# Kernel optimization log

Measured on AMD Instinct MI355X. Metric: run time of the kernel, lower is better.

The kernel has to match this reference:

```python
import jax, jax.numpy as jnp
import numpy as np

N_NODES = 100000
N_EDGES = 3200000
ALPHA = 0.1
ITERATIONS = 10


def setup_inputs() -> dict:
    key = jax.random.key(0)
    ks = jax.random.split(key, 7)
    features = jax.random.normal(ks[0], (N_NODES, 512), dtype=jnp.float32)
    W1 = jax.random.normal(ks[1], (512, 64), dtype=jnp.float32) * 0.05
    b1 = jax.random.normal(ks[2], (64,), dtype=jnp.float32) * 0.05
    W2 = jax.random.normal(ks[3], (64, 64), dtype=jnp.float32) * 0.05
    b2 = jax.random.normal(ks[4], (64,), dtype=jnp.float32) * 0.05
    edge_weights = jax.random.uniform(ks[5], (N_EDGES,), dtype=jnp.float32)
    edge_index = jax.random.randint(ks[6], (2, N_EDGES), 0, N_NODES, dtype=jnp.int64)
    return {"features": features, "W1": W1, "b1": b1, "W2": W2, "b2": b2,
            "edge_weights": edge_weights, "edge_index": edge_index}


def reference(features, W1, b1, W2, b2, edge_weights, edge_index):
    # dense MLP head (dropout disabled / eval mode)
    h = jax.nn.relu(features @ W1 + b1)          # [N, hidden]
    z = h @ W2 + b2                              # [N, labels]

    row, col = edge_index[0], edge_index[1]

    def step(p, _):
        # SpMM: out[row] += w * p[col]
        gathered = edge_weights[:, None] * p[col]                 # [E, labels]
        new = jax.ops.segment_sum(gathered, row, num_segments=N_NODES)
        p = (1.0 - ALPHA) * new + ALPHA * z
        return p, None

    p, _ = jax.lax.scan(step, z, None, length=ITERATIONS)
    return p
```

## Files before the change

kernel.cpp:

```cpp
#include <hip/hip_runtime.h>
#include <hip/hip_fp16.h>
#include <cmath>

#define N_NODES 100000
#define N_EDGES 3200000
#define ALPHA   0.1f
#define ITERS   10
#define NBUK    1024
#define RPB     98
#define CHUNK   8192
#define NCH     391

typedef __attribute__((ext_vector_type(8))) short short8;
typedef __attribute__((ext_vector_type(4))) float f32x4;

__device__ __forceinline__ short f2bf(float x) {
    union { float f; unsigned u; } v; v.f = x;
    unsigned r = v.u + 0x7fffu + ((v.u >> 16) & 1u);
    return (short)(r >> 16);
}

__global__ void prep_w(const float* __restrict__ W1, const float* __restrict__ W2,
                       short* __restrict__ W1t, short* __restrict__ W2t)
{
    int t = blockIdx.x * 256 + threadIdx.x;
    if (t < 512 * 64) { int k = t >> 6, c = t & 63; W1t[c * 512 + k] = f2bf(W1[t]); }
    if (t < 64 * 64)  { int k = t >> 6, c = t & 63; W2t[c * 64 + k]  = f2bf(W2[t]); }
}

__global__ __launch_bounds__(128) void mlp_mfma(
    const float* __restrict__ F, const short* __restrict__ W1t,
    const short* __restrict__ W2t, const float* __restrict__ b1,
    const float* __restrict__ b2, __half* __restrict__ q0)
{
    __shared__ short Ft[32 * 128];
    __shared__ short Ht[32 * 64];

    const int t  = threadIdx.x;
    const int l  = t & 63;
    const int wv = t >> 6;
    const int wr = wv * 16;
    const long base = (long)blockIdx.x * 32;

    const int sr = t >> 2;
    const int ck = (t & 3) * 32;

    float4 f0, f1, f2, f3, f4, f5, f6, f7;

#define LOAD_TILE(kt) do {                                                   \
    const float* p_ = F + (base + sr) * 512 + (kt) * 128 + ck;               \
    f0 = *(const float4*)(p_ +  0);  f1 = *(const float4*)(p_ +  4);         \
    f2 = *(const float4*)(p_ +  8);  f3 = *(const float4*)(p_ + 12);         \
    f4 = *(const float4*)(p_ + 16);  f5 = *(const float4*)(p_ + 20);         \
    f6 = *(const float4*)(p_ + 24);  f7 = *(const float4*)(p_ + 28);         \
} while (0)

#define STORE_PAIR(j2, fa, fb) do {                                          \
    int k_ = ck + (j2) * 8;                                                  \
    short8 s_ = { f2bf((fa).x), f2bf((fa).y), f2bf((fa).z), f2bf((fa).w),    \
                  f2bf((fb).x), f2bf((fb).y), f2bf((fb).z), f2bf((fb).w) };  \
    *(short8*)&Ft[(sr * 128 + k_) ^ ((sr & 7) << 3)] = s_;                   \
} while (0)

    LOAD_TILE(0);

    f32x4 acc[4] = {};
    for (int kt = 0; kt < 4; ++kt) {
        STORE_PAIR(0, f0, f1);
        STORE_PAIR(1, f2, f3);
        STORE_PAIR(2, f4, f5);
        STORE_PAIR(3, f6, f7);
        __syncthreads();
        if (kt < 3) LOAD_TILE(kt + 1);
#pragma unroll
        for (int kc = 0; kc < 4; ++kc) {
            int kb = kc * 32 + (l >> 4) * 8;
            int ar = wr + (l & 15);
            short8 a = *(const short8*)&Ft[(ar * 128 + kb) ^ ((ar & 7) << 3)];
#pragma unroll
            for (int n = 0; n < 4; ++n) {
                int bc = n * 16 + (l & 15);
                short8 b = *(const short8*)(W1t + bc * 512 + kt * 128 + kb);
                acc[n] = __builtin_amdgcn_mfma_f32_16x16x32_bf16(a, b, acc[n], 0, 0, 0);
            }
        }
        __syncthreads();
    }

#pragma unroll
    for (int n = 0; n < 4; ++n) {
        int col = n * 16 + (l & 15);
        float bv = b1[col];
#pragma unroll
        for (int i = 0; i < 4; ++i) {
            int row = wr + (l >> 4) * 4 + i;
            float hv = fmaxf(acc[n][i] + bv, 0.0f);
            Ht[(row * 64 + col) ^ ((row & 7) << 3)] = f2bf(hv);
        }
    }
    f32x4 acc2[4] = {};
#pragma unroll
    for (int kc = 0; kc < 2; ++kc) {
        int kb = kc * 32 + (l >> 4) * 8;
        int ar = wr + (l & 15);
        short8 a = *(const short8*)&Ht[(ar * 64 + kb) ^ ((ar & 7) << 3)];
#pragma unroll
        for (int n = 0; n < 4; ++n) {
            int bc = n * 16 + (l & 15);
            short8 b = *(const short8*)(W2t + bc * 64 + kb);
            acc2[n] = __builtin_amdgcn_mfma_f32_16x16x32_bf16(a, b, acc2[n], 0, 0, 0);
        }
    }
#pragma unroll
    for (int n = 0; n < 4; ++n) {
        int col = n * 16 + (l & 15);
        float bv = b2[col];
#pragma unroll
        for (int i = 0; i < 4; ++i) {
            long row = base + wr + (l >> 4) * 4 + i;
            q0[row * 64 + col] = __float2half(acc2[n][i] + bv);
        }
    }
#undef LOAD_TILE
#undef STORE_PAIR
}

__global__ __launch_bounds__(256) void bhist(const int* __restrict__ rows, int* __restrict__ gh)
{
    __shared__ int cnt[NBUK];
    for (int i = threadIdx.x; i < NBUK; i += 256) cnt[i] = 0;
    __syncthreads();
    int base = blockIdx.x * CHUNK;
    int end  = base + CHUNK; if (end > N_EDGES) end = N_EDGES;
    for (int i = base + threadIdx.x; i < end; i += 256)
        atomicAdd(&cnt[rows[i] / RPB], 1);
    __syncthreads();
    for (int i = threadIdx.x; i < NBUK; i += 256)
        gh[i * NCH + blockIdx.x] = cnt[i];
}

__global__ __launch_bounds__(512) void bscan(int* __restrict__ gh, int* __restrict__ btot)
{
    __shared__ int s[512];
    int k = blockIdx.x;
    int t = threadIdx.x;
    int v = (t < NCH) ? gh[k * NCH + t] : 0;
    s[t] = v;
    __syncthreads();
    for (int off = 1; off < 512; off <<= 1) {
        int x = (t >= off) ? s[t - off] : 0;
        __syncthreads();
        s[t] += x;
        __syncthreads();
    }
    if (t < NCH) gh[k * NCH + t] = s[t] - v;
    if (t == NCH - 1) btot[k] = s[t];
}

__global__ __launch_bounds__(1024) void scan_btot(const int* __restrict__ btot, int* __restrict__ bbase)
{
    __shared__ int s[1024];
    int t = threadIdx.x;
    int v = btot[t];
    s[t] = v;
    __syncthreads();
    for (int off = 1; off < 1024; off <<= 1) {
        int x = (t >= off) ? s[t - off] : 0;
        __syncthreads();
        s[t] += x;
        __syncthreads();
    }
    bbase[t] = s[t] - v;
}

__global__ __launch_bounds__(256) void bpart(const int* __restrict__ rows, const int* __restrict__ cols,
                                             const float* __restrict__ w, const int* __restrict__ gh,
                                             const int* __restrict__ bbase, uint2* __restrict__ stg)
{
    __shared__ int cur[NBUK];
    int blk = blockIdx.x;
    for (int i = threadIdx.x; i < NBUK; i += 256)
        cur[i] = bbase[i] + gh[i * NCH + blk];
    __syncthreads();
    int base = blk * CHUNK;
    int end  = base + CHUNK; if (end > N_EDGES) end = N_EDGES;
    for (int i = base + threadIdx.x; i < end; i += 256) {
        int r = rows[i];
        int b = r / RPB;
        int pos = atomicAdd(&cur[b], 1);
        float ws = w[i] * ((1.0f - ALPHA) / 16.0f);
        unsigned meta = (unsigned)cols[i] | ((unsigned)(r - b * RPB) << 17);
        stg[pos] = make_uint2(meta, __float_as_uint(ws));
    }
}

__global__ __launch_bounds__(256) void bucket_sort2(const int* __restrict__ bbase,
                                                    const uint2* __restrict__ stg,
                                                    unsigned long long* __restrict__ cw,
                                                    int* __restrict__ rowp)
{
    __shared__ int ldeg[RPB];
    __shared__ int lcur[RPB];
    __shared__ int sc[128];
    const int b = blockIdx.x;
    const int rowlo = b * RPB;
    if (rowlo >= N_NODES) return;
    int rowhi = rowlo + RPB; if (rowhi > N_NODES) rowhi = N_NODES;
    const int nrows = rowhi - rowlo;
    const int t = threadIdx.x;
    const int base = bbase[b];
    const int cnt = ((b + 1 < NBUK) ? bbase[b + 1] : N_EDGES) - base;

    if (t < RPB) ldeg[t] = 0;
    __syncthreads();
    for (int j = t; j < cnt; j += 256)
        atomicAdd(&ldeg[stg[base + j].x >> 17], 1);
    __syncthreads();
    int v = 0;
    if (t < 128) { v = (t < nrows) ? ldeg[t] : 0; sc[t] = v; }
    __syncthreads();
    for (int off = 1; off < 128; off <<= 1) {
        int x = (t < 128 && t >= off) ? sc[t - off] : 0;
        __syncthreads();
        if (t < 128) sc[t] += x;
        __syncthreads();
    }
    if (t < nrows) {
        int rp = base + sc[t] - v;
        rowp[rowlo + t] = rp;
        lcur[t] = rp;
    }
    if (t == 0 && rowhi == N_NODES) rowp[N_NODES] = base + cnt;
    __syncthreads();
    for (int j = t; j < cnt; j += 256) {
        uint2 rec = stg[base + j];
        int roff = rec.x >> 17;
        unsigned col = rec.x & 0x1FFFFu;
        int pos = atomicAdd(&lcur[roff], 1);
        cw[pos] = (unsigned long long)col | ((unsigned long long)rec.y << 32);
    }
}

template <int LAST>
__global__ __launch_bounds__(256) void spmm_kernel(
    const int* __restrict__ rowp, const unsigned long long* __restrict__ cw,
    const __half* __restrict__ qin, const __half* __restrict__ zh,
    float beta, float outscale,
    __half* __restrict__ qout, float* __restrict__ out)
{
    const int wid = blockIdx.x * 4 + (threadIdx.x >> 6);
    if (wid >= N_NODES) return;
    const int lane = threadIdx.x & 63;
    const int sub  = lane >> 3;
    const int l8   = lane & 7;

    const int start = rowp[wid];
    const int end   = rowp[wid + 1];

    uint4 zv = *(const uint4*)(zh + (long)wid * 64 + l8 * 8);

    float a0 = 0, a1 = 0, a2 = 0, a3 = 0, a4 = 0, a5 = 0, a6 = 0, a7 = 0;

#define ACC_EDGE(pc, v)                                                       \
    do {                                                                      \
        float ww_ = __uint_as_float((unsigned)((pc) >> 32));                  \
        float2 p_;                                                            \
        p_ = __half22float2(*(__half2*)&(v).x); a0 += ww_ * p_.x; a1 += ww_ * p_.y; \
        p_ = __half22float2(*(__half2*)&(v).y); a2 += ww_ * p_.x; a3 += ww_ * p_.y; \
        p_ = __half22float2(*(__half2*)&(v).z); a4 += ww_ * p_.x; a5 += ww_ * p_.y; \
        p_ = __half22float2(*(__half2*)&(v).w); a6 += ww_ * p_.x; a7 += ww_ * p_.y; \
    } while (0)

    int e = start + sub;
    for (; e + 8 < end; e += 16) {
        unsigned long long pc0 = cw[e];
        unsigned long long pc1 = cw[e + 8];
        uint4 v0 = *(const uint4*)(qin + (long)(unsigned)pc0 * 64 + l8 * 8);
        uint4 v1 = *(const uint4*)(qin + (long)(unsigned)pc1 * 64 + l8 * 8);
        ACC_EDGE(pc0, v0);
        ACC_EDGE(pc1, v1);
    }
    if (e < end) {
        unsigned long long pc = cw[e];
        uint4 v = *(const uint4*)(qin + (long)(unsigned)pc * 64 + l8 * 8);
        ACC_EDGE(pc, v);
    }
#undef ACC_EDGE

    a0 += __shfl_xor(a0, 8);  a1 += __shfl_xor(a1, 8);
    a2 += __shfl_xor(a2, 8);  a3 += __shfl_xor(a3, 8);
    a4 += __shfl_xor(a4, 8);  a5 += __shfl_xor(a5, 8);
    a6 += __shfl_xor(a6, 8);  a7 += __shfl_xor(a7, 8);
    a0 += __shfl_xor(a0, 16); a1 += __shfl_xor(a1, 16);
    a2 += __shfl_xor(a2, 16); a3 += __shfl_xor(a3, 16);
    a4 += __shfl_xor(a4, 16); a5 += __shfl_xor(a5, 16);
    a6 += __shfl_xor(a6, 16); a7 += __shfl_xor(a7, 16);
    a0 += __shfl_xor(a0, 32); a1 += __shfl_xor(a1, 32);
    a2 += __shfl_xor(a2, 32); a3 += __shfl_xor(a3, 32);
    a4 += __shfl_xor(a4, 32); a5 += __shfl_xor(a5, 32);
    a6 += __shfl_xor(a6, 32); a7 += __shfl_xor(a7, 32);

    if (lane < 8) {
        float2 z0 = __half22float2(*(__half2*)&zv.x);
        float2 z1 = __half22float2(*(__half2*)&zv.y);
        float2 z2 = __half22float2(*(__half2*)&zv.z);
        float2 z3 = __half22float2(*(__half2*)&zv.w);
        float o0 = a0 + beta * z0.x, o1 = a1 + beta * z0.y;
        float o2 = a2 + beta * z1.x, o3 = a3 + beta * z1.y;
        float o4 = a4 + beta * z2.x, o5 = a5 + beta * z2.y;
        float o6 = a6 + beta * z3.x, o7 = a7 + beta * z3.y;
        if (LAST) {
            float4 ra = { outscale * o0, outscale * o1, outscale * o2, outscale * o3 };
            float4 rb = { outscale * o4, outscale * o5, outscale * o6, outscale * o7 };
            *(float4*)(out + (long)wid * 64 + lane * 8)     = ra;
            *(float4*)(out + (long)wid * 64 + lane * 8 + 4) = rb;
        } else {
            __half2 h0 = __floats2half2_rn(o0, o1);
            __half2 h1 = __floats2half2_rn(o2, o3);
            __half2 h2 = __floats2half2_rn(o4, o5);
            __half2 h3 = __floats2half2_rn(o6, o7);
            uint4 pv = { *(unsigned*)&h0, *(unsigned*)&h1, *(unsigned*)&h2, *(unsigned*)&h3 };
            *(uint4*)(qout + (long)wid * 64 + lane * 8) = pv;
        }
    }
}

extern "C" void kernel_launch(void* const* d_in, const int* in_sizes, int n_in,
                              void* d_out, int out_size, void* d_ws, size_t ws_size,
                              hipStream_t stream)
{
    const float* features = (const float*)d_in[0];
    const float* W1 = (const float*)d_in[1];
    const float* b1 = (const float*)d_in[2];
    const float* W2 = (const float*)d_in[3];
    const float* b2 = (const float*)d_in[4];
    const float* ew = (const float*)d_in[5];
    const int*   ei = (const int*)d_in[6];
    const int* erow = ei;
    const int* ecol = ei + N_EDGES;
    float* out = (float*)d_out;

    char* ws = (char*)d_ws;
    size_t off = 0;
    auto alloc = [&](size_t bytes) {
        size_t c = off;
        off += (bytes + 255) & ~(size_t)255;
        return c;
    };
    __half* q0    = (__half*)(ws + alloc((size_t)N_NODES * 64 * 2));
    __half* qA    = (__half*)(ws + alloc((size_t)N_NODES * 64 * 2));
    __half* qB    = (__half*)(ws + alloc((size_t)N_NODES * 64 * 2));
    unsigned long long* cw = (unsigned long long*)(ws + alloc((size_t)N_EDGES * 8));
    uint2* stg    = (uint2*)(ws + alloc((size_t)N_EDGES * 8));
    int*   gh     = (int*)  (ws + alloc((size_t)NBUK * NCH * 4));
    short* W1t    = (short*)(ws + alloc((size_t)512 * 64 * 2));
    short* W2t    = (short*)(ws + alloc((size_t)64 * 64 * 2));
    int*   rowp   = (int*)  (ws + alloc((size_t)(N_NODES + 1) * 4));
    int*   btot   = (int*)  (ws + alloc((size_t)NBUK * 4));
    int*   bbase  = (int*)  (ws + alloc((size_t)NBUK * 4));
    (void)ws_size; (void)in_sizes; (void)n_in; (void)out_size;

    prep_w<<<128, 256, 0, stream>>>(W1, W2, W1t, W2t);
    mlp_mfma<<<N_NODES / 32, 128, 0, stream>>>(features, W1t, W2t, b1, b2, q0);

    bhist<<<NCH, 256, 0, stream>>>(erow, gh);
    bscan<<<NBUK, 512, 0, stream>>>(gh, btot);
    scan_btot<<<1, 1024, 0, stream>>>(btot, bbase);
    bpart<<<NCH, 256, 0, stream>>>(erow, ecol, ew, gh, bbase, stg);
    bucket_sort2<<<NBUK, 256, 0, stream>>>(bbase, stg, cw, rowp);

    const __half* qi = q0;
    for (int it = 1; it < ITERS; ++it) {
        __half* qo = (it & 1) ? qA : qB;
        float beta = (float)(0.1 / pow(16.0, (double)it));
        spmm_kernel<0><<<(N_NODES + 3) / 4, 256, 0, stream>>>(rowp, cw, qi, q0, beta, 1.0f, qo, nullptr);
        qi = qo;
    }
    float beta10 = (float)(0.1 / pow(16.0, 10.0));
    float osc    = (float)pow(16.0, 10.0);
    spmm_kernel<1><<<(N_NODES + 3) / 4, 256, 0, stream>>>(rowp, cw, qi, q0, beta10, osc, nullptr, out);
}
```

Baseline: 772.3 us.

## Split each row's edges into column-range chunks for gather locality

The bucket sort now orders each row's edges by one of four column ranges and stores per-row chunk lengths. The SpMM kernel walks the four segments in turn, so concurrent waves gather from similar regions of the feature matrix and cache reuse may improve. In exchange, each row pays four loop prologues and tails and an extra per-row metadata load.

```diff
diff --git a/kernel.cpp b/kernel.cpp
--- a/kernel.cpp
+++ b/kernel.cpp
@@ -10,6 +10,7 @@
 #define RPB     98
 #define CHUNK   8192
 #define NCH     391
+#define CCH     25000
 
 typedef __attribute__((ext_vector_type(8))) short short8;
 typedef __attribute__((ext_vector_type(4))) float f32x4;
@@ -194,13 +195,14 @@
     }
 }
 
-__global__ __launch_bounds__(256) void bucket_sort2(const int* __restrict__ bbase,
+__global__ __launch_bounds__(256) void bucket_sort3(const int* __restrict__ bbase,
                                                     const uint2* __restrict__ stg,
                                                     unsigned long long* __restrict__ cw,
-                                                    int* __restrict__ rowp)
-{
-    __shared__ int ldeg[RPB];
-    __shared__ int lcur[RPB];
+                                                    int* __restrict__ rowp,
+                                                    uint2* __restrict__ rowlen)
+{
+    __shared__ int ldeg[RPB * 4];
+    __shared__ int lcur[RPB * 4];
     __shared__ int sc[128];
     const int b = blockIdx.x;
     const int rowlo = b * RPB;
@@ -211,13 +213,20 @@
     const int base = bbase[b];
     const int cnt = ((b + 1 < NBUK) ? bbase[b + 1] : N_EDGES) - base;
 
-    if (t < RPB) ldeg[t] = 0;
-    __syncthreads();
-    for (int j = t; j < cnt; j += 256)
-        atomicAdd(&ldeg[stg[base + j].x >> 17], 1);
+    for (int i = t; i < RPB * 4; i += 256) ldeg[i] = 0;
+    __syncthreads();
+    for (int j = t; j < cnt; j += 256) {
+        unsigned x = stg[base + j].x;
+        int roff = x >> 17;
+        int ch = (int)((x & 0x1FFFFu) / CCH);
+        atomicAdd(&ldeg[roff * 4 + ch], 1);
+    }
     __syncthreads();
     int v = 0;
-    if (t < 128) { v = (t < nrows) ? ldeg[t] : 0; sc[t] = v; }
+    if (t < 128) {
+        v = (t < nrows) ? (ldeg[t * 4] + ldeg[t * 4 + 1] + ldeg[t * 4 + 2] + ldeg[t * 4 + 3]) : 0;
+        sc[t] = v;
+    }
     __syncthreads();
     for (int off = 1; off < 128; off <<= 1) {
         int x = (t < 128 && t >= off) ? sc[t - off] : 0;
@@ -228,7 +237,13 @@
     if (t < nrows) {
         int rp = base + sc[t] - v;
         rowp[rowlo + t] = rp;
-        lcur[t] = rp;
+        int c0 = ldeg[t * 4], c1 = ldeg[t * 4 + 1], c2 = ldeg[t * 4 + 2], c3 = ldeg[t * 4 + 3];
+        lcur[t * 4]     = rp;
+        lcur[t * 4 + 1] = rp + c0;
+        lcur[t * 4 + 2] = rp + c0 + c1;
+        lcur[t * 4 + 3] = rp + c0 + c1 + c2;
+        rowlen[rowlo + t] = make_uint2((unsigned)c0 | ((unsigned)c1 << 16),
+                                       (unsigned)c2 | ((unsigned)c3 << 16));
     }
     if (t == 0 && rowhi == N_NODES) rowp[N_NODES] = base + cnt;
     __syncthreads();
@@ -236,14 +251,16 @@
         uint2 rec = stg[base + j];
         int roff = rec.x >> 17;
         unsigned col = rec.x & 0x1FFFFu;
-        int pos = atomicAdd(&lcur[roff], 1);
+        int ch = (int)(col / CCH);
+        int pos = atomicAdd(&lcur[roff * 4 + ch], 1);
         cw[pos] = (unsigned long long)col | ((unsigned long long)rec.y << 32);
     }
 }
 
 template <int LAST>
 __global__ __launch_bounds__(256) void spmm_kernel(
-    const int* __restrict__ rowp, const unsigned long long* __restrict__ cw,
+    const int* __restrict__ rowp, const uint2* __restrict__ rowlen,
+    const unsigned long long* __restrict__ cw,
     const __half* __restrict__ qin, const __half* __restrict__ zh,
     float beta, float outscale,
     __half* __restrict__ qout, float* __restrict__ out)
@@ -255,7 +272,10 @@
     const int l8   = lane & 7;
 
     const int start = rowp[wid];
-    const int end   = rowp[wid + 1];
+    const uint2 rl  = rowlen[wid];
+    const int len0 = rl.x & 0xFFFF, len1 = rl.x >> 16;
+    const int len2 = rl.y & 0xFFFF, len3 = rl.y >> 16;
+    const int s1 = start + len0, s2 = s1 + len1, s3 = s2 + len2, e3 = s3 + len3;
 
     uint4 zv = *(const uint4*)(zh + (long)wid * 64 + l8 * 8);
 
@@ -271,20 +291,29 @@
         p_ = __half22float2(*(__half2*)&(v).w); a6 += ww_ * p_.x; a7 += ww_ * p_.y; \
     } while (0)
 
-    int e = start + sub;
-    for (; e + 8 < end; e += 16) {
-        unsigned long long pc0 = cw[e];
-        unsigned long long pc1 = cw[e + 8];
-        uint4 v0 = *(const uint4*)(qin + (long)(unsigned)pc0 * 64 + l8 * 8);
-        uint4 v1 = *(const uint4*)(qin + (long)(unsigned)pc1 * 64 + l8 * 8);
-        ACC_EDGE(pc0, v0);
-        ACC_EDGE(pc1, v1);
-    }
-    if (e < end) {
-        unsigned long long pc = cw[e];
-        uint4 v = *(const uint4*)(qin + (long)(unsigned)pc * 64 + l8 * 8);
-        ACC_EDGE(pc, v);
-    }
+#define DO_SEG(S, E)                                                          \
+    do {                                                                      \
+        int e = (S) + sub;                                                    \
+        for (; e + 8 < (E); e += 16) {                                        \
+            unsigned long long pc0 = cw[e];                                   \
+            unsigned long long pc1 = cw[e + 8];                               \
+            uint4 v0 = *(const uint4*)(qin + (long)(unsigned)pc0 * 64 + l8 * 8); \
+            uint4 v1 = *(const uint4*)(qin + (long)(unsigned)pc1 * 64 + l8 * 8); \
+            ACC_EDGE(pc0, v0);                                                \
+            ACC_EDGE(pc1, v1);                                                \
+        }                                                                     \
+        if (e < (E)) {                                                        \
+            unsigned long long pc = cw[e];                                    \
+            uint4 v = *(const uint4*)(qin + (long)(unsigned)pc * 64 + l8 * 8); \
+            ACC_EDGE(pc, v);                                                  \
+        }                                                                     \
+    } while (0)
+
+    DO_SEG(start, s1);
+    DO_SEG(s1, s2);
+    DO_SEG(s2, s3);
+    DO_SEG(s3, e3);
+#undef DO_SEG
 #undef ACC_EDGE
 
     a0 += __shfl_xor(a0, 8);  a1 += __shfl_xor(a1, 8);
@@ -356,6 +385,7 @@
     short* W1t    = (short*)(ws + alloc((size_t)512 * 64 * 2));
     short* W2t    = (short*)(ws + alloc((size_t)64 * 64 * 2));
     int*   rowp   = (int*)  (ws + alloc((size_t)(N_NODES + 1) * 4));
+    uint2* rowlen = (uint2*)(ws + alloc((size_t)N_NODES * 8));
     int*   btot   = (int*)  (ws + alloc((size_t)NBUK * 4));
     int*   bbase  = (int*)  (ws + alloc((size_t)NBUK * 4));
     (void)ws_size; (void)in_sizes; (void)n_in; (void)out_size;
@@ -367,16 +397,16 @@
     bscan<<<NBUK, 512, 0, stream>>>(gh, btot);
     scan_btot<<<1, 1024, 0, stream>>>(btot, bbase);
     bpart<<<NCH, 256, 0, stream>>>(erow, ecol, ew, gh, bbase, stg);
-    bucket_sort2<<<NBUK, 256, 0, stream>>>(bbase, stg, cw, rowp);
+    bucket_sort3<<<NBUK, 256, 0, stream>>>(bbase, stg, cw, rowp, rowlen);
 
     const __half* qi = q0;
     for (int it = 1; it < ITERS; ++it) {
         __half* qo = (it & 1) ? qA : qB;
         float beta = (float)(0.1 / pow(16.0, (double)it));
-        spmm_kernel<0><<<(N_NODES + 3) / 4, 256, 0, stream>>>(rowp, cw, qi, q0, beta, 1.0f, qo, nullptr);
+        spmm_kernel<0><<<(N_NODES + 3) / 4, 256, 0, stream>>>(rowp, rowlen, cw, qi, q0, beta, 1.0f, qo, nullptr);
         qi = qo;
     }
     float beta10 = (float)(0.1 / pow(16.0, 10.0));
     float osc    = (float)pow(16.0, 10.0);
-    spmm_kernel<1><<<(N_NODES + 3) / 4, 256, 0, stream>>>(rowp, cw, qi, q0, beta10, osc, nullptr, out);
-}
+    spmm_kernel<1><<<(N_NODES + 3) / 4, 256, 0, stream>>>(rowp, rowlen, cw, qi, q0, beta10, osc, nullptr, out);
+}
```

After: 981.3 us. +27.1%, slower.
